# Kernel tuning notes

Measured on AMD Instinct MI355X. Metric: run time of the kernel, lower is better.

Reference implementation:

```python
import jax, jax.numpy as jnp
import numpy as np

B, S, D, H, DK, L, DFF, V = 64, 128, 512, 8, 64, 6, 2048, 72
AH = 2          # heads of the internal mask-generating attention encoder (hard-coded n_heads=2)
PRECET = 0.2    # fraction of lowest-attention prefix tokens to mask
NEG = -1e9


def pos_enc(s, d):
    pos = jnp.arange(s, dtype=jnp.float32)[:, None]
    div = jnp.exp(jnp.arange(0, d, 2, dtype=jnp.float32) * (-np.log(10000.0) / d))
    pe = jnp.zeros((s, d), jnp.float32)
    pe = pe.at[:, 0::2].set(jnp.sin(pos * div))
    pe = pe.at[:, 1::2].set(jnp.cos(pos * div))
    return pe


def ln(x, eps=1e-5):  # LayerNorm with default (identity) affine params, as in the source
    m = x.mean(-1, keepdims=True)
    v = ((x - m) ** 2).mean(-1, keepdims=True)
    return (x - m) / jnp.sqrt(v + eps)


def attn_block(x, pad, WQ, WK, WV, WO, heads):
    b, s, _ = x.shape
    dk = WQ.shape[1] // heads
    q = (x @ WQ).reshape(b, s, heads, dk).transpose(0, 2, 1, 3)
    k = (x @ WK).reshape(b, s, heads, dk).transpose(0, 2, 1, 3)
    v = (x @ WV).reshape(b, s, heads, dk).transpose(0, 2, 1, 3)
    scores = jnp.einsum('bhqd,bhkd->bhqk', q, k) / np.sqrt(dk)
    scores = jnp.where(pad[:, None, None, :], NEG, scores)
    attn = jax.nn.softmax(scores, axis=-1)
    ascore = attn.sum(axis=2)                                   # [b, h, s] column sums
    ctx = jnp.einsum('bhqk,bhkd->bqhd', attn, v).reshape(b, s, heads * dk)
    return ln(ctx @ WO + x), attn, ascore


def ffn_block(x, W1, W2):
    return ln(jax.nn.relu(x @ W1) @ W2 + x)


def encode(x, pad, tWQ, tWK, tWV, tFC, tF1, tF2):
    def step(h, p):
        WQ, WK, WV, WO, W1, W2 = p
        h, _, asc = attn_block(h, pad, WQ, WK, WV, WO, H)
        h = ffn_block(h, W1, W2)
        return h, asc.sum(axis=1)                               # sum over heads -> [b, s]
    h, scores = jax.lax.scan(step, x, (tWQ, tWK, tWV, tFC, tF1, tF2))
    return h, scores                                            # scores: [L, b, s]


def creat_mask(col, tokens):
    # col[i, j] == 0 exactly iff token j is pad (softmax of -1e9 underflows to 0).
    b, s = tokens.shape
    iszero = col == 0.0
    has = iszero.any(axis=1)
    j0 = jnp.where(has, jnp.argmax(iszero, axis=1), s)          # first pad position
    kk = jnp.where(has, jnp.ceil(PRECET * j0.astype(jnp.float32)).astype(jnp.int32), 0)
    idx = jnp.arange(s)
    vals = jnp.where(idx[None, :] < j0[:, None], col, jnp.inf)
    ranks = jnp.argsort(jnp.argsort(vals, axis=1), axis=1)      # rank 0 = smallest attention
    keep = (ranks >= kk[:, None]).astype(tokens.dtype)
    return tokens * keep


def pre_head(x, pW1, pb1, pW2, pb2, pW3, pb3):
    x = jax.nn.relu(x @ pW1 + pb1)
    x = jax.nn.relu(x @ pW2 + pb2)
    return x @ pW3 + pb3


def setup_inputs():
    key = jax.random.key(0)
    ks = jax.random.split(key, 18)
    g = lambda k, shp: jax.random.normal(k, shp, jnp.float32) * 0.02
    return {
        'tokens': jax.random.randint(ks[0], (B, S), 0, V, dtype=jnp.int32),
        'emb': g(ks[1], (V, D)),
        'aWQ': g(ks[2], (D, AH * DK)), 'aWK': g(ks[3], (D, AH * DK)), 'aWV': g(ks[4], (D, AH * DK)),
        'aFC': g(ks[5], (AH * DK, D)), 'aF1': g(ks[6], (D, DFF)), 'aF2': g(ks[7], (DFF, D)),
        'tWQ': g(ks[8], (L, D, H * DK)), 'tWK': g(ks[9], (L, D, H * DK)), 'tWV': g(ks[10], (L, D, H * DK)),
        'tFC': g(ks[11], (L, H * DK, D)), 'tF1': g(ks[12], (L, D, DFF)), 'tF2': g(ks[13], (L, DFF, D)),
        'pW1': g(ks[14], (D * S, 1024)), 'pb1': jnp.zeros((1024,), jnp.float32),
        'pW2': g(ks[15], (1024, 512)), 'pb2': jnp.zeros((512,), jnp.float32),
        'pW3': g(ks[16], (512, 128)), 'pb3': jnp.zeros((128,), jnp.float32),
    }


def reference(tokens, emb, aWQ, aWK, aWV, aFC, aF1, aF2,
              tWQ, tWK, tWV, tFC, tF1, tF2,
              pW1, pb1, pW2, pb2, pW3, pb3):
    pe = pos_enc(S, D)[None]
    pad = tokens == 0
    x = emb[tokens] + pe
    # 1-layer / 2-head mask-generating encoder; only its attn matrix is consumed downstream
    _, mattn, _ = attn_block(x, pad, aWQ, aWK, aWV, aFC, AH)
    col = mattn.sum(axis=1).sum(axis=1)                         # heads then queries -> [B, S]
    mtok = creat_mask(col, tokens)
    xm = emb[mtok] + pe
    h, scores = encode(x, pad, tWQ, tWK, tWV, tFC, tF1, tF2)
    hm, _ = encode(xm, mtok == 0, tWQ, tWK, tWV, tFC, tF1, tF2)
    out1 = pre_head(h.reshape(B, -1), pW1, pb1, pW2, pb2, pW3, pb3)
    outm = pre_head(hm.reshape(B, -1), pW1, pb1, pW2, pb2, pW3, pb3)
    return tokens, out1, mtok, outm, scores
```

## Files before the change

kernel.cpp:

```cpp
#include <hip/hip_runtime.h>
#include <hip/hip_bf16.h>
#include <math.h>

using u16 = unsigned short;
using u32 = unsigned int;

constexpr int B   = 64;
constexpr int S   = 128;
constexpr int D   = 512;
constexpr int H   = 8;
constexpr int DK  = 64;
constexpr int L   = 6;
constexpr int DFF = 2048;
constexpr int AH  = 2;
constexpr int BS  = B * S;
constexpr int BS2 = 2 * BS;

constexpr long OUT_TOK    = 0;
constexpr long OUT_OUT1   = 8192;
constexpr long OUT_MTOK   = 16384;
constexpr long OUT_OUTM   = 24576;
constexpr long OUT_SCORES = 32768;

constexpr long OFF_PE   = 0;
constexpr long OFF_ASC  = 65536;
constexpr long OFF_COLP = 196608;
constexpr long OFF_MTOK = 212992;
constexpr long OFF_X    = 221184;
constexpr long OFF_XB   = 8609792;
constexpr long OFF_QB   = 12804096;
constexpr long OFF_KB   = 16998400;
constexpr long OFF_VB   = 21192704;
constexpr long OFF_TB   = 25387008;
constexpr long OFF_W    = 42164224;
constexpr long WSTRIDE  = 3145728;

typedef __attribute__((ext_vector_type(8))) short bf16x8;
typedef __attribute__((ext_vector_type(4))) float f32x4;

__device__ __forceinline__ float b2f(u16 u) {
    union { u32 i; float f; } v; v.i = ((u32)u) << 16; return v.f;
}
__device__ __forceinline__ u16 f2b(float f) {
    union { float f; u32 i; } v; v.f = f;
    u32 r = v.i + 0x7fffu + ((v.i >> 16) & 1u);
    return (u16)(r >> 16);
}

#define GLOAD_LDS16(g, l) __builtin_amdgcn_global_load_lds(                        \
    (const __attribute__((address_space(1))) u32*)(const void*)(g),               \
    (__attribute__((address_space(3))) u32*)(void*)(l), 16, 0, 0)

__global__ void pe_kernel(float* __restrict__ pe) {
    int idx = blockIdx.x * 256 + threadIdx.x;
    if (idx >= S * (D / 2)) return;
    int s = idx >> 8;
    int i = idx & 255;
    const float CPE = (float)(-9.210340371976184 / 512.0);
    float div = expf((float)(2 * i) * CPE);
    float ang = (float)s * div;
    pe[(long)s * D + 2 * i]     = sinf(ang);
    pe[(long)s * D + 2 * i + 1] = cosf(ang);
}

__global__ void embed_dual(const int* __restrict__ toks, const float* __restrict__ emb,
                           const float* __restrict__ pe, float* __restrict__ x,
                           u16* __restrict__ xb) {
    int i8 = blockIdx.x * 256 + threadIdx.x;
    if (i8 >= BS * D / 8) return;
    int row = i8 >> 6;
    int c8  = i8 & 63;
    int s   = row & (S - 1);
    int t   = toks[row];
    float4 e0 = *(const float4*)(emb + (long)t * D + c8 * 8);
    float4 e1 = *(const float4*)(emb + (long)t * D + c8 * 8 + 4);
    float4 p0 = *(const float4*)(pe + (long)s * D + c8 * 8);
    float4 p1 = *(const float4*)(pe + (long)s * D + c8 * 8 + 4);
    float4 o0, o1;
    o0.x = e0.x + p0.x; o0.y = e0.y + p0.y; o0.z = e0.z + p0.z; o0.w = e0.w + p0.w;
    o1.x = e1.x + p1.x; o1.y = e1.y + p1.y; o1.z = e1.z + p1.z; o1.w = e1.w + p1.w;
    *(float4*)(x + (long)i8 * 8)     = o0;
    *(float4*)(x + (long)i8 * 8 + 4) = o1;
    u16 u[8] = {f2b(o0.x), f2b(o0.y), f2b(o0.z), f2b(o0.w), f2b(o1.x), f2b(o1.y), f2b(o1.z), f2b(o1.w)};
    *(uint4*)(xb + (long)i8 * 8) = *(uint4*)u;
}

__global__ __launch_bounds__(256)
void wconv_all(const float* __restrict__ tWQ, const float* __restrict__ tWK,
               const float* __restrict__ tWV, const float* __restrict__ tFC,
               const float* __restrict__ tF1, const float* __restrict__ tF2,
               u16* __restrict__ wAll) {
    __shared__ float t[32][33];
    const int lyr = blockIdx.x / 3072;
    const int bid = blockIdx.x % 3072;
    u16* base = wAll + (long)lyr * WSTRIDE;
    const float* src; u16* dst; int KK, NN, tk, tn;
    if (bid < 1024) {
        int which = bid >> 8, tt = bid & 255;
        src = (which == 0 ? tWQ : which == 1 ? tWK : which == 2 ? tWV : tFC) + (long)lyr * D * D;
        dst = base + (long)which * 262144;
        KK = 512; NN = 512; tk = tt >> 4; tn = tt & 15;
    } else if (bid < 2048) {
        int tt = bid - 1024;
        src = tF1 + (long)lyr * D * DFF; dst = base + 1048576;
        KK = 512; NN = 2048; tk = tt >> 6; tn = tt & 63;
    } else {
        int tt = bid - 2048;
        src = tF2 + (long)lyr * DFF * D; dst = base + 2097152;
        KK = 2048; NN = 512; tk = tt >> 4; tn = tt & 15;
    }
    int ty = threadIdx.x >> 5, tx = threadIdx.x & 31;
    #pragma unroll
    for (int i = 0; i < 4; i++)
        t[ty + i * 8][tx] = src[(long)(tk * 32 + ty + i * 8) * NN + tn * 32 + tx];
    __syncthreads();
    #pragma unroll
    for (int i = 0; i < 4; i++)
        dst[(long)(tn * 32 + ty + i * 8) * KK + tk * 32 + tx] = f2b(t[tx][ty + i * 8]);
}

template<int EPI, int OUTB>
__device__ __forceinline__ void gemm_core(
        const u16* __restrict__ A, const u16* __restrict__ Wt,
        float* C, u16* Cb, const void* __restrict__ X,
        int M, int N, int K, int m0, int n0) {
    __shared__ u16 As[2][128 * 32];
    __shared__ u16 Bs[2][128 * 32];
    const int tid = threadIdx.x;
    const int w = tid >> 6, l = tid & 63;
    const int wr = (w >> 1) * 64, wc = (w & 1) * 64;
    f32x4 acc[4][4];
    #pragma unroll
    for (int i = 0; i < 4; i++)
        #pragma unroll
        for (int j = 0; j < 4; j++) { f32x4 z = {0.f, 0.f, 0.f, 0.f}; acc[i][j] = z; }

    const int srow = w * 32 + (l >> 2);
    const int scol = (l & 3) * 8;
    const u16* gA = A + (long)(m0 + srow) * K + scol;
    const u16* gB = Wt + (long)(n0 + srow) * K + scol;

    for (int k0 = 0; k0 < K; k0 += 64) {
        #pragma unroll
        for (int p = 0; p < 2; p++) {
            GLOAD_LDS16(gA + k0 + p * 32,               As[p] + w * 1024);
            GLOAD_LDS16(gA + (long)16 * K + k0 + p * 32, As[p] + w * 1024 + 512);
            GLOAD_LDS16(gB + k0 + p * 32,               Bs[p] + w * 1024);
            GLOAD_LDS16(gB + (long)16 * K + k0 + p * 32, Bs[p] + w * 1024 + 512);
        }
        __syncthreads();
        #pragma unroll
        for (int p = 0; p < 2; p++) {
            bf16x8 aF[4], bF[4];
            #pragma unroll
            for (int mi = 0; mi < 4; mi++)
                aF[mi] = *(const bf16x8*)(As[p] + (wr + mi * 16 + (l & 15)) * 32 + (l >> 4) * 8);
            #pragma unroll
            for (int ni = 0; ni < 4; ni++)
                bF[ni] = *(const bf16x8*)(Bs[p] + (wc + ni * 16 + (l & 15)) * 32 + (l >> 4) * 8);
            #pragma unroll
            for (int mi = 0; mi < 4; mi++)
                #pragma unroll
                for (int ni = 0; ni < 4; ni++)
                    acc[mi][ni] = __builtin_amdgcn_mfma_f32_16x16x32_bf16(aF[mi], bF[ni], acc[mi][ni], 0, 0, 0);
        }
        __syncthreads();
    }

    #pragma unroll
    for (int mi = 0; mi < 4; mi++) {
        #pragma unroll
        for (int ni = 0; ni < 4; ni++) {
            const int col = n0 + wc + ni * 16 + (l & 15);
            #pragma unroll
            for (int r = 0; r < 4; r++) {
                const int row = m0 + wr + mi * 16 + (l >> 4) * 4 + r;
                const long idx = (long)row * N + col;
                float v = acc[mi][ni][r];
                if (EPI == 3) v += b2f(((const u16*)X)[idx]);
                if (EPI == 2) v = fmaxf(v, 0.0f);
                if (OUTB) Cb[idx] = f2b(v);
                else      C[idx]  = v;
            }
        }
    }
}

__global__ __launch_bounds__(256)
void gemm_qkv_b(const u16* __restrict__ A, const u16* wq, const u16* wk, const u16* wv,
                u16* qb, u16* kb, u16* vb, int M, int N, int K) {
    const u16* Wt = blockIdx.z == 0 ? wq : blockIdx.z == 1 ? wk : wv;
    u16* Cb       = blockIdx.z == 0 ? qb : blockIdx.z == 1 ? kb : vb;
    gemm_core<0, 1>(A, Wt, nullptr, Cb, nullptr, M, N, K, blockIdx.x * 128, blockIdx.y * 128);
}
__global__ __launch_bounds__(256)
void gemm_resid_b(const u16* __restrict__ A, const u16* __restrict__ Wt,
                  float* C, const u16* __restrict__ X, int M, int N, int K) {
    gemm_core<3, 0>(A, Wt, C, nullptr, X, M, N, K, blockIdx.x * 128, blockIdx.y * 128);
}
__global__ __launch_bounds__(256)
void gemm_relu_b(const u16* __restrict__ A, const u16* __restrict__ Wt,
                 u16* Cb, int M, int N, int K) {
    gemm_core<2, 1>(A, Wt, nullptr, Cb, nullptr, M, N, K, blockIdx.x * 128, blockIdx.y * 128);
}

template<int EPI>
__global__ __launch_bounds__(256)
void gemm64(const float* __restrict__ A, const float* __restrict__ W,
            float* C, const float* X, int M, int N, int K) {
    __shared__ float As[32][68];
    __shared__ float Ws[32][64];
    const int m0 = blockIdx.x * 64, n0 = blockIdx.y * 64;
    const int tid  = threadIdx.x;
    const int tr   = tid >> 4, tc = tid & 15;
    const int arow = tid >> 3, acg = tid & 7;
    const int wrow = tid >> 4, wcg = tid & 15;
    float acc[4][4] = {};
    for (int k0 = 0; k0 < K; k0 += 32) {
        float4 a0 = *(const float4*)(A + (long)(m0 + arow) * K + k0 + acg * 4);
        float4 a1 = *(const float4*)(A + (long)(m0 + arow + 32) * K + k0 + acg * 4);
        float4 w0 = *(const float4*)(W + (long)(k0 + wrow) * N + n0 + wcg * 4);
        float4 w1 = *(const float4*)(W + (long)(k0 + wrow + 16) * N + n0 + wcg * 4);
        As[acg * 4 + 0][arow] = a0.x; As[acg * 4 + 1][arow] = a0.y;
        As[acg * 4 + 2][arow] = a0.z; As[acg * 4 + 3][arow] = a0.w;
        As[acg * 4 + 0][arow + 32] = a1.x; As[acg * 4 + 1][arow + 32] = a1.y;
        As[acg * 4 + 2][arow + 32] = a1.z; As[acg * 4 + 3][arow + 32] = a1.w;
        *(float4*)&Ws[wrow][wcg * 4]      = w0;
        *(float4*)&Ws[wrow + 16][wcg * 4] = w1;
        __syncthreads();
        #pragma unroll
        for (int kk = 0; kk < 32; kk++) {
            float4 av = *(const float4*)&As[kk][tr * 4];
            float4 bv = *(const float4*)&Ws[kk][tc * 4];
            acc[0][0] += av.x * bv.x; acc[0][1] += av.x * bv.y; acc[0][2] += av.x * bv.z; acc[0][3] += av.x * bv.w;
            acc[1][0] += av.y * bv.x; acc[1][1] += av.y * bv.y; acc[1][2] += av.y * bv.z; acc[1][3] += av.y * bv.w;
            acc[2][0] += av.z * bv.x; acc[2][1] += av.z * bv.y; acc[2][2] += av.z * bv.z; acc[2][3] += av.z * bv.w;
            acc[3][0] += av.w * bv.x; acc[3][1] += av.w * bv.y; acc[3][2] += av.w * bv.z; acc[3][3] += av.w * bv.w;
        }
        __syncthreads();
    }
    #pragma unroll
    for (int i = 0; i < 4; i++) {
        int row = m0 + tr * 4 + i;
        #pragma unroll
        for (int j = 0; j < 4; j++) {
            int col = n0 + tc * 4 + j;
            long idx = (long)row * N + col;
            float v = acc[i][j];
            if (EPI == 1) v += X[idx];
            if (EPI == 3 || EPI == 4) v += X[col];
            if (EPI == 2 || EPI == 4) v = fmaxf(v, 0.0f);
            C[idx] = v;
        }
    }
}

__global__ __launch_bounds__(256)
void gemm64_qkv(const float* __restrict__ A,
                const float* __restrict__ WQ, const float* __restrict__ WK, const float* __restrict__ WV,
                float* q, float* k, float* v, int M, int N, int K) {
    __shared__ float As[32][68];
    __shared__ float Ws[32][64];
    const float* W = (blockIdx.z == 0) ? WQ : (blockIdx.z == 1) ? WK : WV;
    float*       C = (blockIdx.z == 0) ? q  : (blockIdx.z == 1) ? k  : v;
    const int m0 = blockIdx.x * 64, n0 = blockIdx.y * 64;
    const int tid  = threadIdx.x;
    const int tr   = tid >> 4, tc = tid & 15;
    const int arow = tid >> 3, acg = tid & 7;
    const int wrow = tid >> 4, wcg = tid & 15;
    float acc[4][4] = {};
    for (int k0 = 0; k0 < K; k0 += 32) {
        float4 a0 = *(const float4*)(A + (long)(m0 + arow) * K + k0 + acg * 4);
        float4 a1 = *(const float4*)(A + (long)(m0 + arow + 32) * K + k0 + acg * 4);
        float4 w0 = *(const float4*)(W + (long)(k0 + wrow) * N + n0 + wcg * 4);
        float4 w1 = *(const float4*)(W + (long)(k0 + wrow + 16) * N + n0 + wcg * 4);
        As[acg * 4 + 0][arow] = a0.x; As[acg * 4 + 1][arow] = a0.y;
        As[acg * 4 + 2][arow] = a0.z; As[acg * 4 + 3][arow] = a0.w;
        As[acg * 4 + 0][arow + 32] = a1.x; As[acg * 4 + 1][arow + 32] = a1.y;
        As[acg * 4 + 2][arow + 32] = a1.z; As[acg * 4 + 3][arow + 32] = a1.w;
        *(float4*)&Ws[wrow][wcg * 4]      = w0;
        *(float4*)&Ws[wrow + 16][wcg * 4] = w1;
        __syncthreads();
        #pragma unroll
        for (int kk = 0; kk < 32; kk++) {
            float4 av = *(const float4*)&As[kk][tr * 4];
            float4 bv = *(const float4*)&Ws[kk][tc * 4];
            acc[0][0] += av.x * bv.x; acc[0][1] += av.x * bv.y; acc[0][2] += av.x * bv.z; acc[0][3] += av.x * bv.w;
            acc[1][0] += av.y * bv.x; acc[1][1] += av.y * bv.y; acc[1][2] += av.y * bv.z; acc[1][3] += av.y * bv.w;
            acc[2][0] += av.z * bv.x; acc[2][1] += av.z * bv.y; acc[2][2] += av.z * bv.z; acc[2][3] += av.z * bv.w;
            acc[3][0] += av.w * bv.x; acc[3][1] += av.w * bv.y; acc[3][2] += av.w * bv.z; acc[3][3] += av.w * bv.w;
        }
        __syncthreads();
    }
    #pragma unroll
    for (int i = 0; i < 4; i++)
        #pragma unroll
        for (int j = 0; j < 4; j++)
            C[(long)(m0 + tr * 4 + i) * N + n0 + tc * 4 + j] = acc[i][j];
}

__global__ __launch_bounds__(256)
void gemm_ph1(const u16* __restrict__ Ah, const u16* __restrict__ Ahm,
              const float* __restrict__ W, float* __restrict__ P, int KC) {
    constexpr int N = 1024, K = 65536;
    __shared__ u16 As[128 * 32];
    __shared__ u16 Bs[128 * 32];
    const int n0 = blockIdx.x * 128;
    const int kbeg = blockIdx.y * KC;
    const int tid = threadIdx.x;
    const int w = tid >> 6, l = tid & 63;
    const int wr = w * 32;
    const int nl = tid >> 1, seg = tid & 1;
    const u16* aptr = (nl < 64 ? Ah + (long)nl * K : Ahm + (long)(nl - 64) * K) + seg * 16;
    const float* wcol = W + n0 + nl;

    f32x4 acc[2][8];
    #pragma unroll
    for (int mi = 0; mi < 2; mi++)
        #pragma unroll
        for (int ni = 0; ni < 8; ni++) { f32x4 z = {0.f, 0.f, 0.f, 0.f}; acc[mi][ni] = z; }

    for (int ks = 0; ks < KC; ks += 32) {
        const int k0 = kbeg + ks;
        uint4 a0 = *(const uint4*)(aptr + k0);
        uint4 a1 = *(const uint4*)(aptr + k0 + 8);
        float wv[16];
        #pragma unroll
        for (int j = 0; j < 16; j++)
            wv[j] = wcol[(long)(k0 + seg * 16 + j) * N];
        __syncthreads();
        *(uint4*)(As + nl * 32 + seg * 16)     = a0;
        *(uint4*)(As + nl * 32 + seg * 16 + 8) = a1;
        u32 pk[8];
        #pragma unroll
        for (int j = 0; j < 8; j++)
            pk[j] = (u32)f2b(wv[2 * j]) | ((u32)f2b(wv[2 * j + 1]) << 16);
        *(uint4*)(Bs + nl * 32 + seg * 16)     = *(uint4*)&pk[0];
        *(uint4*)(Bs + nl * 32 + seg * 16 + 8) = *(uint4*)&pk[4];
        __syncthreads();
        bf16x8 aF0 = *(const bf16x8*)(As + (wr + (l & 15)) * 32 + (l >> 4) * 8);
        bf16x8 aF1 = *(const bf16x8*)(As + (wr + 16 + (l & 15)) * 32 + (l >> 4) * 8);
        #pragma unroll
        for (int ni = 0; ni < 8; ni++) {
            bf16x8 bF = *(const bf16x8*)(Bs + (ni * 16 + (l & 15)) * 32 + (l >> 4) * 8);
            acc[0][ni] = __builtin_amdgcn_mfma_f32_16x16x32_bf16(aF0, bF, acc[0][ni], 0, 0, 0);
            acc[1][ni] = __builtin_amdgcn_mfma_f32_16x16x32_bf16(aF1, bF, acc[1][ni], 0, 0, 0);
        }
    }
    float* Pz = P + (long)blockIdx.y * 128 * N;
    #pragma unroll
    for (int mi = 0; mi < 2; mi++)
        #pragma unroll
        for (int ni = 0; ni < 8; ni++) {
            const int col = n0 + ni * 16 + (l & 15);
            #pragma unroll
            for (int r = 0; r < 4; r++)
                Pz[(long)(wr + mi * 16 + (l >> 4) * 4 + r) * N + col] = acc[mi][ni][r];
        }
}

__global__ __launch_bounds__(128)
void attn_kernel(const float* __restrict__ Q, const float* __restrict__ K,
                 const int* __restrict__ toks, float* __restrict__ colsum, int Hn) {
    __shared__ float sc[S][129];
    __shared__ float KV[S][DK];
    __shared__ int   padS[S];
    const int b = blockIdx.x / Hn;
    const int h = blockIdx.x % Hn;
    const int stride = Hn * DK;
    const int tid = threadIdx.x;

    for (int idx = tid; idx < S * DK; idx += 128) {
        int r = idx >> 6, c = idx & 63;
        KV[r][c] = K[(long)(b * S + r) * stride + h * DK + c];
    }
    padS[tid] = (toks[b * S + tid] == 0) ? 1 : 0;
    float qreg[DK];
    {
        const float* qp = Q + (long)(b * S + tid) * stride + h * DK;
        #pragma unroll
        for (int i = 0; i < 16; i++) {
            float4 t4 = *(const float4*)(qp + i * 4);
            qreg[i * 4 + 0] = t4.x; qreg[i * 4 + 1] = t4.y;
            qreg[i * 4 + 2] = t4.z; qreg[i * 4 + 3] = t4.w;
        }
    }
    __syncthreads();
    for (int k = 0; k < S; k++) {
        float s = 0.0f;
        #pragma unroll
        for (int d4 = 0; d4 < 16; d4++) {
            float4 kv = *(const float4*)&KV[k][d4 * 4];
            s += qreg[d4 * 4 + 0] * kv.x + qreg[d4 * 4 + 1] * kv.y
               + qreg[d4 * 4 + 2] * kv.z + qreg[d4 * 4 + 3] * kv.w;
        }
        sc[tid][k] = padS[k] ? -1e9f : (s * 0.125f);
    }
    float mx = -INFINITY;
    for (int k = 0; k < S; k++) mx = fmaxf(mx, sc[tid][k]);
    float sum = 0.0f;
    for (int k = 0; k < S; k++) { float e = expf(sc[tid][k] - mx); sc[tid][k] = e; sum += e; }
    for (int k = 0; k < S; k++) sc[tid][k] = sc[tid][k] / sum;
    __syncthreads();
    {
        double a = 0.0;
        for (int q2 = 0; q2 < S; q2++) a += (double)sc[q2][tid];
        colsum[(long)(b * Hn + h) * S + tid] = (float)a;
    }
}

__global__ __launch_bounds__(256)
void attn_mfma_kernel(u16* qb, const u16* __restrict__ kb, const u16* __restrict__ vb,
                      const int* __restrict__ toks, const int* __restrict__ mtok,
                      float* __restrict__ colsum) {
    __shared__ u16 pool[18432];
    __shared__ u16 Vt[64 * 136];
    __shared__ float colsLds[4][128];
    __shared__ u32 padF[128];
    u16* Qs = pool;
    u16* Ks = pool + 9216;
    u16* Ps = pool;

    const int gb = blockIdx.x >> 3, h = blockIdx.x & 7;
    const int tid = threadIdx.x;
    const int w = tid >> 6, l = tid & 63;
    const long base = (long)gb * S * D + h * 64;
    const int* tsrc = (gb < B) ? (toks + (long)gb * S) : (mtok + (long)(gb - B) * S);

    for (int j = tid; j < 1024; j += 256) {
        int r = j >> 3, c = j & 7;
        uint4 uq = *(const uint4*)(qb + base + (long)r * D + c * 8);
        uint4 uk = *(const uint4*)(kb + base + (long)r * D + c * 8);
        uint4 uv = *(const uint4*)(vb + base + (long)r * D + c * 8);
        *(uint4*)(Qs + r * 72 + c * 8) = uq;
        *(uint4*)(Ks + r * 72 + c * 8) = uk;
        u16 vv[8]; *(uint4*)vv = uv;
        #pragma unroll
        for (int t = 0; t < 8; t++) Vt[(c * 8 + t) * 136 + r] = vv[t];
    }
    if (tid < 128) padF[tid] = (tsrc[tid] == 0) ? 1u : 0u;
    __syncthreads();

    const int rowB = w * 32;
    f32x4 acc[2][8];
    #pragma unroll
    for (int mi = 0; mi < 2; mi++)
        #pragma unroll
        for (int ni = 0; ni < 8; ni++) { f32x4 z = {0.f, 0.f, 0.f, 0.f}; acc[mi][ni] = z; }
    #pragma unroll
    for (int ks = 0; ks < 2; ks++) {
        bf16x8 a0 = *(const bf16x8*)(Qs + (rowB + (l & 15)) * 72 + ks * 32 + (l >> 4) * 8);
        bf16x8 a1 = *(const bf16x8*)(Qs + (rowB + 16 + (l & 15)) * 72 + ks * 32 + (l >> 4) * 8);
        #pragma unroll
        for (int ni = 0; ni < 8; ni++) {
            bf16x8 bv = *(const bf16x8*)(Ks + (ni * 16 + (l & 15)) * 72 + ks * 32 + (l >> 4) * 8);
            acc[0][ni] = __builtin_amdgcn_mfma_f32_16x16x32_bf16(a0, bv, acc[0][ni], 0, 0, 0);
            acc[1][ni] = __builtin_amdgcn_mfma_f32_16x16x32_bf16(a1, bv, acc[1][ni], 0, 0, 0);
        }
    }
    float pf[8];
    #pragma unroll
    for (int ni = 0; ni < 8; ni++) pf[ni] = padF[ni * 16 + (l & 15)] ? 1.0f : 0.0f;
    #pragma unroll
    for (int mi = 0; mi < 2; mi++)
        #pragma unroll
        for (int ni = 0; ni < 8; ni++)
            #pragma unroll
            for (int r = 0; r < 4; r++) {
                float v = acc[mi][ni][r] * 0.125f;
                acc[mi][ni][r] = (pf[ni] != 0.0f) ? -1e9f : v;
            }
    #pragma unroll
    for (int mi = 0; mi < 2; mi++)
        #pragma unroll
        for (int r = 0; r < 4; r++) {
            float m = -INFINITY;
            #pragma unroll
            for (int ni = 0; ni < 8; ni++) m = fmaxf(m, acc[mi][ni][r]);
            m = fmaxf(m, __shfl_xor(m, 1)); m = fmaxf(m, __shfl_xor(m, 2));
            m = fmaxf(m, __shfl_xor(m, 4)); m = fmaxf(m, __shfl_xor(m, 8));
            float s = 0.0f;
            #pragma unroll
            for (int ni = 0; ni < 8; ni++) { float e = expf(acc[mi][ni][r] - m); acc[mi][ni][r] = e; s += e; }
            s += __shfl_xor(s, 1); s += __shfl_xor(s, 2);
            s += __shfl_xor(s, 4); s += __shfl_xor(s, 8);
            float inv = 1.0f / s;
            #pragma unroll
            for (int ni = 0; ni < 8; ni++) acc[mi][ni][r] *= inv;
        }
    float cs[8];
    #pragma unroll
    for (int ni = 0; ni < 8; ni++) {
        float s = 0.0f;
        #pragma unroll
        for (int mi = 0; mi < 2; mi++)
            #pragma unroll
            for (int r = 0; r < 4; r++) s += acc[mi][ni][r];
        s += __shfl_xor(s, 16); s += __shfl_xor(s, 32);
        cs[ni] = s;
    }
    __syncthreads();
    if (l < 16)
        #pragma unroll
        for (int ni = 0; ni < 8; ni++) colsLds[w][ni * 16 + l] = cs[ni];
    #pragma unroll
    for (int mi = 0; mi < 2; mi++)
        #pragma unroll
        for (int ni = 0; ni < 8; ni++)
            #pragma unroll
            for (int r = 0; r < 4; r++)
                Ps[(rowB + mi * 16 + (l >> 4) * 4 + r) * 136 + ni * 16 + (l & 15)] =
                    f2b(acc[mi][ni][r]);
    __syncthreads();
    if (tid < 128) {
        float s = colsLds[0][tid] + colsLds[1][tid] + colsLds[2][tid] + colsLds[3][tid];
        colsum[((long)gb * H + h) * S + tid] = s;
    }
    f32x4 o[2][4];
    #pragma unroll
    for (int mi = 0; mi < 2; mi++)
        #pragma unroll
        for (int n = 0; n < 4; n++) { f32x4 z = {0.f, 0.f, 0.f, 0.f}; o[mi][n] = z; }
    #pragma unroll
    for (int ks = 0; ks < 4; ks++) {
        bf16x8 p0 = *(const bf16x8*)(Ps + (rowB + (l & 15)) * 136 + ks * 32 + (l >> 4) * 8);
        bf16x8 p1 = *(const bf16x8*)(Ps + (rowB + 16 + (l & 15)) * 136 + ks * 32 + (l >> 4) * 8);
        #pragma unroll
        for (int n = 0; n < 4; n++) {
            bf16x8 bv = *(const bf16x8*)(Vt + (n * 16 + (l & 15)) * 136 + ks * 32 + (l >> 4) * 8);
            o[0][n] = __builtin_amdgcn_mfma_f32_16x16x32_bf16(p0, bv, o[0][n], 0, 0, 0);
            o[1][n] = __builtin_amdgcn_mfma_f32_16x16x32_bf16(p1, bv, o[1][n], 0, 0, 0);
        }
    }
    #pragma unroll
    for (int mi = 0; mi < 2; mi++)
        #pragma unroll
        for (int n = 0; n < 4; n++) {
            const int col = n * 16 + (l & 15);
            #pragma unroll
            for (int r = 0; r < 4; r++) {
                const int row = rowB + mi * 16 + (l >> 4) * 4 + r;
                qb[base + (long)row * D + col] = f2b(o[mi][n][r]);
            }
        }
}

__global__ __launch_bounds__(128)
void creat_mask_kernel(const float* __restrict__ colpart, const int* __restrict__ toks,
                       int* __restrict__ mtok, float* __restrict__ out) {
    __shared__ float colS[S];
    __shared__ int   j0s, kks;
    const int b = blockIdx.x, j = threadIdx.x;
    float c = colpart[(long)(b * AH + 0) * S + j] + colpart[(long)(b * AH + 1) * S + j];
    colS[j] = c;
    int tk = toks[b * S + j];
    __syncthreads();
    if (j == 0) {
        int j0 = S;
        for (int i = 0; i < S; i++) if (colS[i] == 0.0f) { j0 = i; break; }
        int kk = (j0 < S) ? (int)ceilf(0.2f * (float)j0) : 0;
        j0s = j0; kks = kk;
    }
    __syncthreads();
    const int j0 = j0s, kk = kks;
    float vj = (j < j0) ? colS[j] : INFINITY;
    int rank = 0;
    for (int i = 0; i < S; i++) {
        float vi = (i < j0) ? colS[i] : INFINITY;
        if (vi < vj || (vi == vj && i < j)) rank++;
    }
    int mt = (rank >= kk) ? tk : 0;
    mtok[b * S + j] = mt;
    out[OUT_TOK + b * S + j]  = (float)tk;
    out[OUT_MTOK + b * S + j] = (float)mt;
}

__global__ __launch_bounds__(256)
void ln_kernel(const float* __restrict__ y, u16* __restrict__ xb) {
    const int row  = blockIdx.x * 4 + (threadIdx.x >> 6);
    const int lane = threadIdx.x & 63;
    const float* r = y + (long)row * D;
    float4 v0 = *(const float4*)(r + lane * 4);
    float4 v1 = *(const float4*)(r + 256 + lane * 4);
    float s = v0.x + v0.y + v0.z + v0.w + v1.x + v1.y + v1.z + v1.w;
    #pragma unroll
    for (int off = 32; off; off >>= 1) s += __shfl_xor(s, off);
    float m = s * (1.0f / 512.0f);
    float d0 = v0.x - m, d1 = v0.y - m, d2 = v0.z - m, d3 = v0.w - m;
    float d4 = v1.x - m, d5 = v1.y - m, d6 = v1.z - m, d7 = v1.w - m;
    float q = d0*d0 + d1*d1 + d2*d2 + d3*d3 + d4*d4 + d5*d5 + d6*d6 + d7*d7;
    #pragma unroll
    for (int off = 32; off; off >>= 1) q += __shfl_xor(q, off);
    float inv = 1.0f / sqrtf(q * (1.0f / 512.0f) + 1e-5f);
    u16* rb = xb + (long)row * D;
    u16 p0[4] = {f2b(d0 * inv), f2b(d1 * inv), f2b(d2 * inv), f2b(d3 * inv)};
    u16 p1[4] = {f2b(d4 * inv), f2b(d5 * inv), f2b(d6 * inv), f2b(d7 * inv)};
    *(uint2*)(rb + lane * 4)       = *(uint2*)p0;
    *(uint2*)(rb + 256 + lane * 4) = *(uint2*)p1;
}

__global__ void score_reduce_kernel(const float* __restrict__ ascorep, float* __restrict__ dst) {
    int idx = blockIdx.x * 256 + threadIdx.x;
    if (idx >= B * S) return;
    int b = idx >> 7, j = idx & 127;
    float s = 0.0f;
    for (int h = 0; h < H; h++) s += ascorep[(long)(b * H + h) * S + j];
    dst[idx] = s;
}

__global__ void reduce1_kernel(const float* __restrict__ parts, const float* __restrict__ b1,
                               float* __restrict__ o) {
    int idx = blockIdx.x * 256 + threadIdx.x;
    if (idx >= 128 * 1024) return;
    float s = 0.0f;
    for (int z = 0; z < 64; z++) s += parts[(long)z * 128 * 1024 + idx];
    s += b1[idx & 1023];
    o[idx] = fmaxf(s, 0.0f);
}

__global__ void pack_out_kernel(const float* __restrict__ ph3, float* __restrict__ out) {
    int idx = blockIdx.x * 256 + threadIdx.x;
    if (idx >= 128 * 128) return;
    int row = idx >> 7, col = idx & 127;
    long base = (row < 64) ? (OUT_OUT1 + (long)row * 128) : (OUT_OUTM + (long)(row - 64) * 128);
    out[base + col] = ph3[idx];
}

extern "C" void kernel_launch(void* const* d_in, const int* in_sizes, int n_in,
                              void* d_out, int out_size, void* d_ws, size_t ws_size,
                              hipStream_t stream) {
    const int*   toks = (const int*)d_in[0];
    const float* emb  = (const float*)d_in[1];
    const float* aWQ  = (const float*)d_in[2];
    const float* aWK  = (const float*)d_in[3];
    const float* tWQ  = (const float*)d_in[8];
    const float* tWK  = (const float*)d_in[9];
    const float* tWV  = (const float*)d_in[10];
    const float* tFC  = (const float*)d_in[11];
    const float* tF1  = (const float*)d_in[12];
    const float* tF2  = (const float*)d_in[13];
    const float* pW1  = (const float*)d_in[14];
    const float* pb1  = (const float*)d_in[15];
    const float* pW2  = (const float*)d_in[16];
    const float* pb2  = (const float*)d_in[17];
    const float* pW3  = (const float*)d_in[18];
    const float* pb3  = (const float*)d_in[19];
    float* out = (float*)d_out;

    float* ws   = (float*)d_ws;
    float* pe   = ws + OFF_PE;
    float* ascp = ws + OFF_ASC;
    float* colp = ws + OFF_COLP;
    int*   mtok = (int*)(ws + OFF_MTOK);
    float* x    = ws + OFF_X;
    u16*   xb   = (u16*)(ws + OFF_XB);
    u16*   qb   = (u16*)(ws + OFF_QB);
    u16*   kb   = (u16*)(ws + OFF_KB);
    u16*   vb   = (u16*)(ws + OFF_VB);
    u16*   tb   = (u16*)(ws + OFF_TB);
    u16*   wAll = (u16*)(ws + OFF_W);

    float* maq   = ws + OFF_TB;
    float* mak   = maq + (long)BS * 128;
    float* parts = ws + OFF_TB;
    float* ph1o  = parts + 8388608;
    float* ph2o  = ph1o + 131072;
    float* ph3o  = ph2o + 65536;

    pe_kernel<<<128, 256, 0, stream>>>(pe);
    wconv_all<<<6 * 3072, 256, 0, stream>>>(tWQ, tWK, tWV, tFC, tF1, tF2, wAll);
    embed_dual<<<2048, 256, 0, stream>>>(toks, emb, pe, x, xb);

    gemm64_qkv<<<dim3(BS / 64, 2, 2), 256, 0, stream>>>(
        x, aWQ, aWK, nullptr, maq, mak, nullptr, BS, AH * DK, D);
    attn_kernel<<<B * AH, 128, 0, stream>>>(maq, mak, toks, colp, AH);
    creat_mask_kernel<<<B, 128, 0, stream>>>(colp, toks, mtok, out);
    embed_dual<<<2048, 256, 0, stream>>>(mtok, emb, pe, x + (long)BS * D, xb + (long)BS * D);

    for (int l = 0; l < L; l++) {
        const u16* wq = wAll + (long)l * WSTRIDE;
        const u16* wk = wq + 262144;
        const u16* wv = wq + 524288;
        const u16* wo = wq + 786432;
        const u16* w1 = wq + 1048576;
        const u16* w2 = wq + 2097152;
        gemm_qkv_b<<<dim3(BS2 / 128, D / 128, 3), 256, 0, stream>>>(
            xb, wq, wk, wv, qb, kb, vb, BS2, D, D);
        attn_mfma_kernel<<<2 * B * H, 256, 0, stream>>>(qb, kb, vb, toks, mtok, ascp);
        score_reduce_kernel<<<32, 256, 0, stream>>>(ascp, out + OUT_SCORES + (long)l * BS);
        gemm_resid_b<<<dim3(BS2 / 128, D / 128), 256, 0, stream>>>(qb, wo, x, xb, BS2, D, D);
        ln_kernel<<<BS2 / 4, 256, 0, stream>>>(x, xb);
        gemm_relu_b<<<dim3(BS2 / 128, DFF / 128), 256, 0, stream>>>(xb, w1, tb, BS2, DFF, D);
        gemm_resid_b<<<dim3(BS2 / 128, D / 128), 256, 0, stream>>>(tb, w2, x, xb, BS2, D, DFF);
        ln_kernel<<<BS2 / 4, 256, 0, stream>>>(x, xb);
    }

    gemm_ph1<<<dim3(8, 64), 256, 0, stream>>>(xb, xb + (long)BS * D, pW1, parts, 1024);
    reduce1_kernel<<<512, 256, 0, stream>>>(parts, pb1, ph1o);
    gemm64<4><<<dim3(2, 8), 256, 0, stream>>>(ph1o, pW2, ph2o, pb2, 128, 512, 1024);
    gemm64<3><<<dim3(2, 2), 256, 0, stream>>>(ph2o, pW3, ph3o, pb3, 128, 128, 512);
    pack_out_kernel<<<64, 256, 0, stream>>>(ph3o, out);
}
```

Baseline: 1.497 ms.

## Store residual GEMM output in bf16 and batch per-layer score reductions

The residual GEMMs now write their pre-LayerNorm sum as bf16 into a separate buffer instead of fp32, and LayerNorm reads bf16 and computes mean and variance in one pass (E[x^2]-m^2). The per-layer head-score reduction kernel is replaced by one kernel after the layer loop, which reads per-layer slices of an enlarged buffer, and the second embedding no longer writes its unused fp32 copy. The aim is less memory traffic and fewer launches. In exchange, the residual sum is rounded to bf16 before LayerNorm and the one-pass variance is less numerically stable.

Result: no change. 1.472 ms (-1.7%).

```diff
diff --git a/kernel.cpp b/kernel.cpp
--- a/kernel.cpp
+++ b/kernel.cpp
@@ -23,17 +23,19 @@
 constexpr long OUT_SCORES = 32768;
 
 constexpr long OFF_PE   = 0;
-constexpr long OFF_ASC  = 65536;
-constexpr long OFF_COLP = 196608;
-constexpr long OFF_MTOK = 212992;
-constexpr long OFF_X    = 221184;
-constexpr long OFF_XB   = 8609792;
-constexpr long OFF_QB   = 12804096;
-constexpr long OFF_KB   = 16998400;
-constexpr long OFF_VB   = 21192704;
-constexpr long OFF_TB   = 25387008;
-constexpr long OFF_W    = 42164224;
+constexpr long OFF_ASCL = 65536;
+constexpr long OFF_COLP = 851968;
+constexpr long OFF_MTOK = 868352;
+constexpr long OFF_X    = 876544;
+constexpr long OFF_XB   = 9265152;
+constexpr long OFF_Y    = 13459456;
+constexpr long OFF_QB   = 17653760;
+constexpr long OFF_KB   = 21848064;
+constexpr long OFF_VB   = 26042368;
+constexpr long OFF_TB   = 30236672;
+constexpr long OFF_W    = 47013888;
 constexpr long WSTRIDE  = 3145728;
+constexpr long ASCL_STRIDE = 131072;
 
 typedef __attribute__((ext_vector_type(8))) short bf16x8;
 typedef __attribute__((ext_vector_type(4))) float f32x4;
@@ -64,7 +66,7 @@
 }
 
 __global__ void embed_dual(const int* __restrict__ toks, const float* __restrict__ emb,
-                           const float* __restrict__ pe, float* __restrict__ x,
+                           const float* __restrict__ pe, float* x,
                            u16* __restrict__ xb) {
     int i8 = blockIdx.x * 256 + threadIdx.x;
     if (i8 >= BS * D / 8) return;
@@ -79,8 +81,10 @@
     float4 o0, o1;
     o0.x = e0.x + p0.x; o0.y = e0.y + p0.y; o0.z = e0.z + p0.z; o0.w = e0.w + p0.w;
     o1.x = e1.x + p1.x; o1.y = e1.y + p1.y; o1.z = e1.z + p1.z; o1.w = e1.w + p1.w;
-    *(float4*)(x + (long)i8 * 8)     = o0;
-    *(float4*)(x + (long)i8 * 8 + 4) = o1;
+    if (x) {
+        *(float4*)(x + (long)i8 * 8)     = o0;
+        *(float4*)(x + (long)i8 * 8 + 4) = o1;
+    }
     u16 u[8] = {f2b(o0.x), f2b(o0.y), f2b(o0.z), f2b(o0.w), f2b(o1.x), f2b(o1.y), f2b(o1.z), f2b(o1.w)};
     *(uint4*)(xb + (long)i8 * 8) = *(uint4*)u;
 }
@@ -122,7 +126,7 @@
 template<int EPI, int OUTB>
 __device__ __forceinline__ void gemm_core(
         const u16* __restrict__ A, const u16* __restrict__ Wt,
-        float* C, u16* Cb, const void* __restrict__ X,
+        float* C, u16* Cb, const u16* __restrict__ X,
         int M, int N, int K, int m0, int n0) {
     __shared__ u16 As[2][128 * 32];
     __shared__ u16 Bs[2][128 * 32];
@@ -177,7 +181,7 @@
                 const int row = m0 + wr + mi * 16 + (l >> 4) * 4 + r;
                 const long idx = (long)row * N + col;
                 float v = acc[mi][ni][r];
-                if (EPI == 3) v += b2f(((const u16*)X)[idx]);
+                if (EPI == 3) v += b2f(X[idx]);
                 if (EPI == 2) v = fmaxf(v, 0.0f);
                 if (OUTB) Cb[idx] = f2b(v);
                 else      C[idx]  = v;
@@ -195,8 +199,8 @@
 }
 __global__ __launch_bounds__(256)
 void gemm_resid_b(const u16* __restrict__ A, const u16* __restrict__ Wt,
-                  float* C, const u16* __restrict__ X, int M, int N, int K) {
-    gemm_core<3, 0>(A, Wt, C, nullptr, X, M, N, K, blockIdx.x * 128, blockIdx.y * 128);
+                  u16* Yb, const u16* __restrict__ X, int M, int N, int K) {
+    gemm_core<3, 1>(A, Wt, nullptr, Yb, X, M, N, K, blockIdx.x * 128, blockIdx.y * 128);
 }
 __global__ __launch_bounds__(256)
 void gemm_relu_b(const u16* __restrict__ A, const u16* __restrict__ Wt,
@@ -576,36 +580,43 @@
 }
 
 __global__ __launch_bounds__(256)
-void ln_kernel(const float* __restrict__ y, u16* __restrict__ xb) {
+void ln_kernel(const u16* __restrict__ y, u16* __restrict__ xb) {
     const int row  = blockIdx.x * 4 + (threadIdx.x >> 6);
     const int lane = threadIdx.x & 63;
-    const float* r = y + (long)row * D;
-    float4 v0 = *(const float4*)(r + lane * 4);
-    float4 v1 = *(const float4*)(r + 256 + lane * 4);
-    float s = v0.x + v0.y + v0.z + v0.w + v1.x + v1.y + v1.z + v1.w;
-    #pragma unroll
-    for (int off = 32; off; off >>= 1) s += __shfl_xor(s, off);
-    float m = s * (1.0f / 512.0f);
-    float d0 = v0.x - m, d1 = v0.y - m, d2 = v0.z - m, d3 = v0.w - m;
-    float d4 = v1.x - m, d5 = v1.y - m, d6 = v1.z - m, d7 = v1.w - m;
-    float q = d0*d0 + d1*d1 + d2*d2 + d3*d3 + d4*d4 + d5*d5 + d6*d6 + d7*d7;
-    #pragma unroll
-    for (int off = 32; off; off >>= 1) q += __shfl_xor(q, off);
-    float inv = 1.0f / sqrtf(q * (1.0f / 512.0f) + 1e-5f);
-    u16* rb = xb + (long)row * D;
-    u16 p0[4] = {f2b(d0 * inv), f2b(d1 * inv), f2b(d2 * inv), f2b(d3 * inv)};
-    u16 p1[4] = {f2b(d4 * inv), f2b(d5 * inv), f2b(d6 * inv), f2b(d7 * inv)};
-    *(uint2*)(rb + lane * 4)       = *(uint2*)p0;
-    *(uint2*)(rb + 256 + lane * 4) = *(uint2*)p1;
-}
-
-__global__ void score_reduce_kernel(const float* __restrict__ ascorep, float* __restrict__ dst) {
+    const u16* r = y + (long)row * D;
+    uint4 u = *(const uint4*)(r + lane * 8);
+    u32 uu[4] = {u.x, u.y, u.z, u.w};
+    float v[8];
+    #pragma unroll
+    for (int t = 0; t < 4; t++) {
+        v[t * 2]     = b2f((u16)(uu[t] & 0xffffu));
+        v[t * 2 + 1] = b2f((u16)(uu[t] >> 16));
+    }
+    float s = 0.0f, q = 0.0f;
+    #pragma unroll
+    for (int t = 0; t < 8; t++) { s += v[t]; q += v[t] * v[t]; }
+    #pragma unroll
+    for (int off = 32; off; off >>= 1) { s += __shfl_xor(s, off); q += __shfl_xor(q, off); }
+    float m   = s * (1.0f / 512.0f);
+    float var = q * (1.0f / 512.0f) - m * m;
+    float inv = 1.0f / sqrtf(var + 1e-5f);
+    u16 o[8];
+    #pragma unroll
+    for (int t = 0; t < 8; t++) o[t] = f2b((v[t] - m) * inv);
+    *(uint4*)(xb + (long)row * D + lane * 8) = *(uint4*)o;
+}
+
+__global__ void score_all_kernel(const float* __restrict__ ascl, float* __restrict__ out) {
     int idx = blockIdx.x * 256 + threadIdx.x;
-    if (idx >= B * S) return;
-    int b = idx >> 7, j = idx & 127;
+    if (idx >= L * B * S) return;
+    int l   = idx / (B * S);
+    int rem = idx - l * (B * S);
+    int b = rem >> 7, j = rem & 127;
+    const float* p = ascl + (long)l * ASCL_STRIDE + (long)b * H * S + j;
     float s = 0.0f;
-    for (int h = 0; h < H; h++) s += ascorep[(long)(b * H + h) * S + j];
-    dst[idx] = s;
+    #pragma unroll
+    for (int h = 0; h < H; h++) s += p[(long)h * S];
+    out[OUT_SCORES + idx] = s;
 }
 
 __global__ void reduce1_kernel(const float* __restrict__ parts, const float* __restrict__ b1,
@@ -649,11 +660,12 @@
 
     float* ws   = (float*)d_ws;
     float* pe   = ws + OFF_PE;
-    float* ascp = ws + OFF_ASC;
+    float* ascl = ws + OFF_ASCL;
     float* colp = ws + OFF_COLP;
     int*   mtok = (int*)(ws + OFF_MTOK);
     float* x    = ws + OFF_X;
     u16*   xb   = (u16*)(ws + OFF_XB);
+    u16*   yb   = (u16*)(ws + OFF_Y);
     u16*   qb   = (u16*)(ws + OFF_QB);
     u16*   kb   = (u16*)(ws + OFF_KB);
     u16*   vb   = (u16*)(ws + OFF_VB);
@@ -675,7 +687,7 @@
         x, aWQ, aWK, nullptr, maq, mak, nullptr, BS, AH * DK, D);
     attn_kernel<<<B * AH, 128, 0, stream>>>(maq, mak, toks, colp, AH);
     creat_mask_kernel<<<B, 128, 0, stream>>>(colp, toks, mtok, out);
-    embed_dual<<<2048, 256, 0, stream>>>(mtok, emb, pe, x + (long)BS * D, xb + (long)BS * D);
+    embed_dual<<<2048, 256, 0, stream>>>(mtok, emb, pe, nullptr, xb + (long)BS * D);
 
     for (int l = 0; l < L; l++) {
         const u16* wq = wAll + (long)l * WSTRIDE;
@@ -686,14 +698,15 @@
         const u16* w2 = wq + 2097152;
         gemm_qkv_b<<<dim3(BS2 / 128, D / 128, 3), 256, 0, stream>>>(
             xb, wq, wk, wv, qb, kb, vb, BS2, D, D);
-        attn_mfma_kernel<<<2 * B * H, 256, 0, stream>>>(qb, kb, vb, toks, mtok, ascp);
-        score_reduce_kernel<<<32, 256, 0, stream>>>(ascp, out + OUT_SCORES + (long)l * BS);
-        gemm_resid_b<<<dim3(BS2 / 128, D / 128), 256, 0, stream>>>(qb, wo, x, xb, BS2, D, D);
-        ln_kernel<<<BS2 / 4, 256, 0, stream>>>(x, xb);
+        attn_mfma_kernel<<<2 * B * H, 256, 0, stream>>>(
+            qb, kb, vb, toks, mtok, ascl + (long)l * ASCL_STRIDE);
+        gemm_resid_b<<<dim3(BS2 / 128, D / 128), 256, 0, stream>>>(qb, wo, yb, xb, BS2, D, D);
+        ln_kernel<<<BS2 / 4, 256, 0, stream>>>(yb, xb);
         gemm_relu_b<<<dim3(BS2 / 128, DFF / 128), 256, 0, stream>>>(xb, w1, tb, BS2, DFF, D);
-        gemm_resid_b<<<dim3(BS2 / 128, D / 128), 256, 0, stream>>>(tb, w2, x, xb, BS2, D, DFF);
-        ln_kernel<<<BS2 / 4, 256, 0, stream>>>(x, xb);
-    }
+        gemm_resid_b<<<dim3(BS2 / 128, D / 128), 256, 0, stream>>>(tb, w2, yb, xb, BS2, D, DFF);
+        ln_kernel<<<BS2 / 4, 256, 0, stream>>>(yb, xb);
+    }
+    score_all_kernel<<<192, 256, 0, stream>>>(ascl, out);
 
     gemm_ph1<<<dim3(8, 64), 256, 0, stream>>>(xb, xb + (long)BS * D, pW1, parts, 1024);
     reduce1_kernel<<<512, 256, 0, stream>>>(parts, pb1, ph1o);
```
